# Kernel tuning notes

Measured on AMD Instinct MI355X. Metric: run time of the kernel, lower is better.

The kernel has to match this reference:

```python
import jax, jax.numpy as jnp
import numpy as np

CE_SLICES = [(1,10),(12,29),(30,33),(33,40),(40,64),(64,79),(79,84),(84,94),(94,96),(96,99),(99,105),(105,113),(116,122),(122,128),(128,151),(151,159),(160,165)]
MSE_COLS = [0,10,11,29,113,114,115,159,165,166,167]
BINS = 800
RATIO_JSD = 0.1  # stand-in for par.RATIO_JSD (not defined in source)
B = 262144


def setup_inputs() -> dict:
    key = jax.random.key(0)
    k1, k2, k3, k4 = jax.random.split(key, 4)
    data_encoded = jax.random.normal(k1, (B, 11), dtype=jnp.float32)
    data_decoded = jax.random.normal(k2, (B, 168), dtype=jnp.float32)
    data_true = jax.random.normal(k3, (B, 168), dtype=jnp.float32)
    # categorical blocks of data_true must be one-hot (nonzero-based decode)
    for j, (s, e) in enumerate(CE_SLICES):
        lab = jax.random.randint(jax.random.fold_in(k3, j), (B,), 0, e - s)
        data_true = data_true.at[:, s:e].set(jax.nn.one_hot(lab, e - s, dtype=jnp.float32))
    label_true = jax.random.randint(k4, (B, 1), 0, 2).astype(jnp.float32)
    return {"data_encoded": data_encoded, "data_decoded": data_decoded,
            "data_true": data_true, "label_true": label_true, "batch_size": B}


def _ce(logits, labels):
    # F.cross_entropy with mean reduction
    logp = jax.nn.log_softmax(logits, axis=-1)
    return -jnp.mean(jnp.take_along_axis(logp, labels[:, None], axis=1))


def _hist(x, mn, mx, mask):
    # torch.histc semantics: BINS equal bins on [mn, mx], top edge inclusive.
    t = (x - mn) / (mx - mn)
    idx = jnp.clip(jnp.floor(t * BINS).astype(jnp.int32), 0, BINS - 1)
    return jax.ops.segment_sum(mask, idx, num_segments=BINS)


def _kl(p, q, eps=1e-12):
    return jnp.sum(jnp.where(p > 0, p * jnp.log((p + eps) / (q + eps)), 0.0))


def reference(data_encoded, data_decoded, data_true, label_true, batch_size):
    # ---- MSE losses over 11 scalar columns (vectorized) ----
    cols = jnp.array(MSE_COLS)
    diff = data_decoded[:, cols] - data_true[:, cols]            # [B, 11]
    mse_loss = jnp.sum(jnp.mean(diff * diff, axis=0))

    # ---- 17 cross-entropy heads (labels decoded from one-hot blocks) ----
    ce_loss = jnp.float32(0.0)
    for s, e in CE_SLICES:
        labels = jnp.argmax(data_true[:, s:e], axis=1)           # == first nonzero for one-hot
        ce_loss = ce_loss + _ce(data_decoded[:, s:e], labels)

    # ---- JSD between male/female histograms of first 10 encoded dims ----
    combined = jnp.concatenate([data_encoded, label_true], axis=1)  # [B, 12]
    mn = jnp.min(combined, axis=0)
    mx = jnp.max(combined, axis=0)
    male = (combined[:, 11] == 0).astype(jnp.float32)
    female = (combined[:, 11] == 1).astype(jnp.float32)
    cols10 = combined[:, :10].T                                  # [10, B]
    hist = jax.vmap(_hist, in_axes=(0, 0, 0, None))              # [10, BINS]
    m_h = hist(cols10, mn[:10], mx[:10], male) / jnp.sum(male)
    f_h = hist(cols10, mn[:10], mx[:10], female) / jnp.sum(female)
    mid = 0.5 * (m_h + f_h)
    kld = 0.5 * (_kl(m_h, mid) + _kl(f_h, mid))                  # Jensen-Shannon divergence

    multi = (1.0 - RATIO_JSD) * (mse_loss + ce_loss) + RATIO_JSD * kld
    return jnp.stack([multi, mse_loss, ce_loss, RATIO_JSD * kld])
```

## Files before the change

### kernel.cpp

```cpp
#include <hip/hip_runtime.h>
#include <math.h>


#define BINS 800
#define NHCOLS 10
#define HBLK 256

#define MIN_OFF 0
#define MAX_OFF 16
#define CNT_OFF 32
#define MH_OFF  64
#define FH_OFF  8064
#define SUM2_OFF 16384
#define SUM2_CE  (SUM2_OFF + 2048)
#define WS_TOTAL_U32 20480

__device__ __forceinline__ unsigned f2ord(float f) {
  unsigned u = __float_as_uint(f);
  return (u & 0x80000000u) ? ~u : (u | 0x80000000u);
}
__device__ __forceinline__ float ord2f(unsigned e) {
  return __uint_as_float((e & 0x80000000u) ? (e & 0x7FFFFFFFu) : ~e);
}

__global__ void k_init(unsigned* __restrict__ ws) {
  int i = blockIdx.x * blockDim.x + threadIdx.x;
  if (i < WS_TOTAL_U32) ws[i] = (i < 11) ? 0xFFFFFFFFu : 0u;
}

__global__ __launch_bounds__(256) void k_minmax(const float* __restrict__ enc,
                                                const float* __restrict__ lab,
                                                unsigned* __restrict__ ws, int B) {
  const int tid    = blockIdx.x * blockDim.x + threadIdx.x;
  const int stride = gridDim.x * blockDim.x;
  const int c      = tid % 11;
  unsigned mn = 0xFFFFFFFFu, mx = 0u;
  const long long total = (long long)B * 11;
  for (long long i = tid; i < total; i += stride) {
    unsigned e = f2ord(enc[i]);
    mn = mn < e ? mn : e;
    mx = mx > e ? mx : e;
  }
  __shared__ unsigned smn[11], smx[11], scnt[2];
  if (threadIdx.x < 11) { smn[threadIdx.x] = 0xFFFFFFFFu; smx[threadIdx.x] = 0u; }
  if (threadIdx.x < 2)  scnt[threadIdx.x] = 0u;
  __syncthreads();
  atomicMin(&smn[c], mn);
  atomicMax(&smx[c], mx);
  unsigned m = 0, f = 0;
  for (int i = tid; i < B; i += stride) {
    float v = lab[i];
    m += (v == 0.0f);
    f += (v == 1.0f);
  }
  atomicAdd(&scnt[0], m);
  atomicAdd(&scnt[1], f);
  __syncthreads();
  if (threadIdx.x < 11) {
    atomicMin(&ws[MIN_OFF + threadIdx.x], smn[threadIdx.x]);
    atomicMax(&ws[MAX_OFF + threadIdx.x], smx[threadIdx.x]);
  }
  if (threadIdx.x == 11) atomicAdd(&ws[CNT_OFF + 0], scnt[0]);
  if (threadIdx.x == 12) atomicAdd(&ws[CNT_OFF + 1], scnt[1]);
}

__global__ __launch_bounds__(256) void k_hist(const float* __restrict__ enc,
                                              const float* __restrict__ lab,
                                              unsigned* __restrict__ ws, int B) {
  __shared__ unsigned h[2][NHCOLS * BINS];
  __shared__ float smn[NHCOLS], srng[NHCOLS];
  unsigned* hf = &h[0][0];
  for (int i = threadIdx.x; i < 2 * NHCOLS * BINS; i += blockDim.x) hf[i] = 0u;
  if (threadIdx.x < NHCOLS) {
    float lo = ord2f(ws[MIN_OFF + threadIdx.x]);
    float hi = ord2f(ws[MAX_OFF + threadIdx.x]);
    smn[threadIdx.x] = lo;
    srng[threadIdx.x] = hi - lo;
  }
  __syncthreads();
  const int sub    = (threadIdx.x >> 6) & 1;
  const int total  = B * 11;
  const int stride = HBLK * 256;
  const int qs     = stride / 11;
  const int rs     = stride % 11;
  int i = blockIdx.x * 256 + threadIdx.x;
  int r = i / 11;
  int c = i - r * 11;
  for (; i < total; i += stride) {
    if (c < NHCOLS) {
      float lv = lab[r];
      unsigned add = (lv == 0.0f) ? 1u : ((lv == 1.0f) ? 0x10000u : 0u);
      if (add) {
        float t = (enc[i] - smn[c]) / srng[c];
        int b = (int)floorf(t * 800.0f);
        b = b < 0 ? 0 : (b > BINS - 1 ? BINS - 1 : b);
        atomicAdd(&h[sub][c * BINS + b], add);
      }
    }
    r += qs; c += rs;
    if (c >= 11) { c -= 11; ++r; }
  }
  __syncthreads();
  for (int k = threadIdx.x; k < NHCOLS * BINS; k += blockDim.x) {
    unsigned v = h[0][k] + h[1][k];
    unsigned m = v & 0xFFFFu, f = v >> 16;
    if (m) atomicAdd(&ws[MH_OFF + k], m);
    if (f) atomicAdd(&ws[FH_OFF + k], f);
  }
}

__host__ __device__ constexpr int slice_of(int c) {
  return (c>=1&&c<10)?0:(c>=12&&c<29)?1:(c>=30&&c<33)?2:(c>=33&&c<40)?3:
         (c>=40&&c<64)?4:(c>=64&&c<79)?5:(c>=79&&c<84)?6:(c>=84&&c<94)?7:
         (c>=94&&c<96)?8:(c>=96&&c<99)?9:(c>=99&&c<105)?10:(c>=105&&c<113)?11:
         (c>=116&&c<122)?12:(c>=122&&c<128)?13:(c>=128&&c<151)?14:
         (c>=151&&c<159)?15:(c>=160&&c<165)?16:-1;
}
__host__ __device__ constexpr bool mse_of(int c) {
  return c==0||c==10||c==11||c==29||c==113||c==114||c==115||c==159||
         c==165||c==166||c==167;
}

template<int I, int K>
__device__ __forceinline__ void elem(const float (&d)[11][4], const float (&t)[11][4],
                                     float (&s)[17], float &dot, float &mse, int j) {
  constexpr int c0 = 16*I + K, c1 = c0+4, c2 = c0+8, c3 = c0+12;
  constexpr int cem = ((c0<168 && slice_of(c0)>=0)?1:0) |
                      ((c1<168 && slice_of(c1)>=0)?2:0) |
                      ((c2<168 && slice_of(c2)>=0)?4:0) |
                      ((c3<168 && slice_of(c3)>=0)?8:0);
  constexpr int msm = ((c0<168 && mse_of(c0))?1:0) | ((c1<168 && mse_of(c1))?2:0) |
                      ((c2<168 && mse_of(c2))?4:0) | ((c3<168 && mse_of(c3))?8:0);
  const float dv = d[I][K], tv = t[I][K];
  if constexpr (cem != 0) {
    float e = __expf(dv);
    if constexpr (cem & 1) s[slice_of(c0)] += (j == 0) ? e : 0.0f;
    if constexpr (cem & 2) s[slice_of(c1)] += (j == 1) ? e : 0.0f;
    if constexpr (cem & 4) s[slice_of(c2)] += (j == 2) ? e : 0.0f;
    if constexpr (cem & 8) s[slice_of(c3)] += (j == 3) ? e : 0.0f;
    dot += ((cem >> j) & 1) ? tv * dv : 0.0f;
  }
  if constexpr (msm != 0) {
    float df = dv - tv;
    mse += ((msm >> j) & 1) ? df * df : 0.0f;
  }
}

template<int I>
__device__ __forceinline__ void elem_row(const float (&d)[11][4], const float (&t)[11][4],
                                         float (&s)[17], float &dot, float &mse, int j) {
  elem<I,0>(d, t, s, dot, mse, j);
  elem<I,1>(d, t, s, dot, mse, j);
  elem<I,2>(d, t, s, dot, mse, j);
  elem<I,3>(d, t, s, dot, mse, j);
}

__global__ __launch_bounds__(256, 3) void k_main(const float* __restrict__ dec,
                                                 const float* __restrict__ tru,
                                                 float* __restrict__ wsf, int B) {
  const int lane = threadIdx.x & 63;
  const int wid  = threadIdx.x >> 6;
  const int j    = lane & 3;
  const int row  = blockIdx.x * 64 + (wid << 4) + (lane >> 2);
  const bool valid = row < B;
  const int rowc = valid ? row : (B - 1);

  float d[11][4], t[11][4];
  const float4* d4 = (const float4*)(dec + (size_t)rowc * 168);
  const float4* t4 = (const float4*)(tru + (size_t)rowc * 168);
#pragma unroll
  for (int i = 0; i < 11; ++i) {
    int w = 4 * i + j;
    w = w > 41 ? 41 : w;
    const float4 dv = d4[w];
    const float4 tv = t4[w];
    d[i][0] = dv.x; d[i][1] = dv.y; d[i][2] = dv.z; d[i][3] = dv.w;
    t[i][0] = tv.x; t[i][1] = tv.y; t[i][2] = tv.z; t[i][3] = tv.w;
  }
#pragma unroll
  for (int i = 0; i < 11; ++i) {
    asm volatile("" : "+v"(d[i][0]), "+v"(d[i][1]), "+v"(d[i][2]), "+v"(d[i][3]),
                      "+v"(t[i][0]), "+v"(t[i][1]), "+v"(t[i][2]), "+v"(t[i][3]));
  }

  float s[17];
#pragma unroll
  for (int k = 0; k < 17; ++k) s[k] = 0.0f;
  float dot = 0.0f, mse = 0.0f;

  elem_row<0>(d, t, s, dot, mse, j);
  elem_row<1>(d, t, s, dot, mse, j);
  elem_row<2>(d, t, s, dot, mse, j);
  elem_row<3>(d, t, s, dot, mse, j);
  elem_row<4>(d, t, s, dot, mse, j);
  elem_row<5>(d, t, s, dot, mse, j);
  elem_row<6>(d, t, s, dot, mse, j);
  elem_row<7>(d, t, s, dot, mse, j);
  elem_row<8>(d, t, s, dot, mse, j);
  elem_row<9>(d, t, s, dot, mse, j);
  elem_row<10>(d, t, s, dot, mse, j);

  dot += __shfl_xor(dot, 1, 64);
  dot += __shfl_xor(dot, 2, 64);
#pragma unroll
  for (int k = 0; k < 17; ++k) {
    s[k] += __shfl_xor(s[k], 1, 64);
    s[k] += __shfl_xor(s[k], 2, 64);
  }
  float ce = -dot;
#pragma unroll
  for (int k = 0; k < 17; ++k) ce += __logf(s[k]);

  ce  = (valid && j == 0) ? ce : 0.0f;
  mse = valid ? mse : 0.0f;

  __shared__ float sm[4], sc[4];
#pragma unroll
  for (int off = 32; off > 0; off >>= 1) {
    mse += __shfl_down(mse, off, 64);
    ce  += __shfl_down(ce, off, 64);
  }
  if (lane == 0) { sm[wid] = mse; sc[wid] = ce; }
  __syncthreads();
  if (threadIdx.x == 0) {
    const int slot = (blockIdx.x & 63) * 32;
    atomicAdd(&wsf[SUM2_OFF + slot], sm[0] + sm[1] + sm[2] + sm[3]);
    atomicAdd(&wsf[SUM2_CE  + slot], sc[0] + sc[1] + sc[2] + sc[3]);
  }
}

__global__ __launch_bounds__(256) void k_final(const unsigned* __restrict__ ws,
                                               float* __restrict__ out, int B) {
  const float* wsf = (const float*)ws;
  float male   = (float)ws[CNT_OFF + 0];
  float female = (float)ws[CNT_OFF + 1];
  float local = 0.0f;
  for (int i = threadIdx.x; i < NHCOLS * BINS; i += blockDim.x) {
    float mh  = (float)ws[MH_OFF + i] / male;
    float fh  = (float)ws[FH_OFF + i] / female;
    float mid = 0.5f * (mh + fh);
    if (mh > 0.0f) local += mh * logf((mh + 1e-12f) / (mid + 1e-12f));
    if (fh > 0.0f) local += fh * logf((fh + 1e-12f) / (mid + 1e-12f));
  }
  int lane = threadIdx.x & 63, wid = threadIdx.x >> 6;
  float msep = 0.0f, cep = 0.0f;
  if (threadIdx.x < 64) {
    msep = wsf[SUM2_OFF + threadIdx.x * 32];
    cep  = wsf[SUM2_CE  + threadIdx.x * 32];
  }
  __shared__ float s[4], sm2, sc2;
#pragma unroll
  for (int off = 32; off > 0; off >>= 1) {
    local += __shfl_down(local, off, 64);
    msep  += __shfl_down(msep, off, 64);
    cep   += __shfl_down(cep, off, 64);
  }
  if (lane == 0) s[wid] = local;
  if (threadIdx.x == 0) { sm2 = msep; sc2 = cep; }
  __syncthreads();
  if (threadIdx.x == 0) {
    float kld   = 0.5f * (s[0] + s[1] + s[2] + s[3]);
    float mse   = sm2 / (float)B;
    float ce    = sc2 / (float)B;
    float multi = 0.9f * (mse + ce) + 0.1f * kld;
    out[0] = multi;
    out[1] = mse;
    out[2] = ce;
    out[3] = 0.1f * kld;
  }
}

extern "C" void kernel_launch(void* const* d_in, const int* in_sizes, int n_in,
                              void* d_out, int out_size, void* d_ws, size_t ws_size,
                              hipStream_t stream) {
  (void)n_in; (void)out_size; (void)ws_size;
  const float* enc = (const float*)d_in[0];
  const float* dec = (const float*)d_in[1];
  const float* tru = (const float*)d_in[2];
  const float* lab = (const float*)d_in[3];
  const int B = in_sizes[3];
  unsigned* ws = (unsigned*)d_ws;
  float* out = (float*)d_out;

  hipLaunchKernelGGL(k_init, dim3((WS_TOTAL_U32 + 255) / 256), dim3(256), 0, stream, ws);
  hipLaunchKernelGGL(k_minmax, dim3(352), dim3(256), 0, stream, enc, lab, ws, B);
  hipLaunchKernelGGL(k_hist, dim3(HBLK), dim3(256), 0, stream, enc, lab, ws, B);
  hipLaunchKernelGGL(k_main, dim3((B + 63) / 64), dim3(256), 0, stream,
                     dec, tru, (float*)ws, B);
  hipLaunchKernelGGL(k_final, dim3(1), dim3(256), 0, stream, ws, out, B);
}
```

Before: 443.0 us.

## Remap main kernel to eight lanes per row and replace init kernel with memset

The main kernel now assigns eight lanes per row instead of four, so each thread holds 6 float4 vectors instead of 11. Column masks are rebuilt with constexpr helpers and the shuffle reductions gain one more stage. Launch bounds are raised to target four blocks per SIMD. The min-reduction is stored as a max over bitwise-inverted values, so an all-zero memset can replace the custom init kernel. The intent is lower register pressure, higher occupancy, more loads in flight, and one fewer kernel launch, at the cost of extra shuffles and more blocks.

After: 439.3 us. About the same (-0.8%).

```diff
diff --git a/kernel.cpp b/kernel.cpp
--- a/kernel.cpp
+++ b/kernel.cpp
@@ -15,17 +15,14 @@
 #define SUM2_CE  (SUM2_OFF + 2048)
 #define WS_TOTAL_U32 20480
 
+typedef float f4 __attribute__((ext_vector_type(4)));
+
 __device__ __forceinline__ unsigned f2ord(float f) {
   unsigned u = __float_as_uint(f);
   return (u & 0x80000000u) ? ~u : (u | 0x80000000u);
 }
 __device__ __forceinline__ float ord2f(unsigned e) {
   return __uint_as_float((e & 0x80000000u) ? (e & 0x7FFFFFFFu) : ~e);
-}
-
-__global__ void k_init(unsigned* __restrict__ ws) {
-  int i = blockIdx.x * blockDim.x + threadIdx.x;
-  if (i < WS_TOTAL_U32) ws[i] = (i < 11) ? 0xFFFFFFFFu : 0u;
 }
 
 __global__ __launch_bounds__(256) void k_minmax(const float* __restrict__ enc,
@@ -34,18 +31,19 @@
   const int tid    = blockIdx.x * blockDim.x + threadIdx.x;
   const int stride = gridDim.x * blockDim.x;
   const int c      = tid % 11;
-  unsigned mn = 0xFFFFFFFFu, mx = 0u;
+  unsigned mni = 0u, mx = 0u;
   const long long total = (long long)B * 11;
   for (long long i = tid; i < total; i += stride) {
     unsigned e = f2ord(enc[i]);
-    mn = mn < e ? mn : e;
-    mx = mx > e ? mx : e;
+    unsigned ei = ~e;
+    mni = mni > ei ? mni : ei;
+    mx  = mx  > e  ? mx  : e;
   }
   __shared__ unsigned smn[11], smx[11], scnt[2];
-  if (threadIdx.x < 11) { smn[threadIdx.x] = 0xFFFFFFFFu; smx[threadIdx.x] = 0u; }
+  if (threadIdx.x < 11) { smn[threadIdx.x] = 0u; smx[threadIdx.x] = 0u; }
   if (threadIdx.x < 2)  scnt[threadIdx.x] = 0u;
   __syncthreads();
-  atomicMin(&smn[c], mn);
+  atomicMax(&smn[c], mni);
   atomicMax(&smx[c], mx);
   unsigned m = 0, f = 0;
   for (int i = tid; i < B; i += stride) {
@@ -57,7 +55,7 @@
   atomicAdd(&scnt[1], f);
   __syncthreads();
   if (threadIdx.x < 11) {
-    atomicMin(&ws[MIN_OFF + threadIdx.x], smn[threadIdx.x]);
+    atomicMax(&ws[MIN_OFF + threadIdx.x], smn[threadIdx.x]);
     atomicMax(&ws[MAX_OFF + threadIdx.x], smx[threadIdx.x]);
   }
   if (threadIdx.x == 11) atomicAdd(&ws[CNT_OFF + 0], scnt[0]);
@@ -72,7 +70,7 @@
   unsigned* hf = &h[0][0];
   for (int i = threadIdx.x; i < 2 * NHCOLS * BINS; i += blockDim.x) hf[i] = 0u;
   if (threadIdx.x < NHCOLS) {
-    float lo = ord2f(ws[MIN_OFF + threadIdx.x]);
+    float lo = ord2f(~ws[MIN_OFF + threadIdx.x]);
     float hi = ord2f(ws[MAX_OFF + threadIdx.x]);
     smn[threadIdx.x] = lo;
     srng[threadIdx.x] = hi - lo;
@@ -120,34 +118,50 @@
   return c==0||c==10||c==11||c==29||c==113||c==114||c==115||c==159||
          c==165||c==166||c==167;
 }
+__host__ __device__ constexpr unsigned cem_of(int base) {
+  unsigned m = 0;
+  for (int jj = 0; jj < 8; ++jj) {
+    int c = base + 4 * jj;
+    if (c < 168 && slice_of(c) >= 0) m |= (1u << jj);
+  }
+  return m;
+}
+__host__ __device__ constexpr unsigned msm_of(int base) {
+  unsigned m = 0;
+  for (int jj = 0; jj < 8; ++jj) {
+    int c = base + 4 * jj;
+    if (c < 168 && mse_of(c)) m |= (1u << jj);
+  }
+  return m;
+}
 
 template<int I, int K>
-__device__ __forceinline__ void elem(const float (&d)[11][4], const float (&t)[11][4],
+__device__ __forceinline__ void elem(const f4 (&d)[6], const f4 (&t)[6],
                                      float (&s)[17], float &dot, float &mse, int j) {
-  constexpr int c0 = 16*I + K, c1 = c0+4, c2 = c0+8, c3 = c0+12;
-  constexpr int cem = ((c0<168 && slice_of(c0)>=0)?1:0) |
-                      ((c1<168 && slice_of(c1)>=0)?2:0) |
-                      ((c2<168 && slice_of(c2)>=0)?4:0) |
-                      ((c3<168 && slice_of(c3)>=0)?8:0);
-  constexpr int msm = ((c0<168 && mse_of(c0))?1:0) | ((c1<168 && mse_of(c1))?2:0) |
-                      ((c2<168 && mse_of(c2))?4:0) | ((c3<168 && mse_of(c3))?8:0);
+  constexpr int base = 32 * I + K;
+  constexpr unsigned cem = cem_of(base);
+  constexpr unsigned msm = msm_of(base);
   const float dv = d[I][K], tv = t[I][K];
   if constexpr (cem != 0) {
     float e = __expf(dv);
-    if constexpr (cem & 1) s[slice_of(c0)] += (j == 0) ? e : 0.0f;
-    if constexpr (cem & 2) s[slice_of(c1)] += (j == 1) ? e : 0.0f;
-    if constexpr (cem & 4) s[slice_of(c2)] += (j == 2) ? e : 0.0f;
-    if constexpr (cem & 8) s[slice_of(c3)] += (j == 3) ? e : 0.0f;
-    dot += ((cem >> j) & 1) ? tv * dv : 0.0f;
+    if constexpr (cem & 1u)   s[slice_of(base + 0)]  += (j == 0) ? e : 0.0f;
+    if constexpr (cem & 2u)   s[slice_of(base + 4)]  += (j == 1) ? e : 0.0f;
+    if constexpr (cem & 4u)   s[slice_of(base + 8)]  += (j == 2) ? e : 0.0f;
+    if constexpr (cem & 8u)   s[slice_of(base + 12)] += (j == 3) ? e : 0.0f;
+    if constexpr (cem & 16u)  s[slice_of(base + 16)] += (j == 4) ? e : 0.0f;
+    if constexpr (cem & 32u)  s[slice_of(base + 20)] += (j == 5) ? e : 0.0f;
+    if constexpr (cem & 64u)  s[slice_of(base + 24)] += (j == 6) ? e : 0.0f;
+    if constexpr (cem & 128u) s[slice_of(base + 28)] += (j == 7) ? e : 0.0f;
+    dot += ((cem >> j) & 1u) ? tv * dv : 0.0f;
   }
   if constexpr (msm != 0) {
     float df = dv - tv;
-    mse += ((msm >> j) & 1) ? df * df : 0.0f;
+    mse += ((msm >> j) & 1u) ? df * df : 0.0f;
   }
 }
 
 template<int I>
-__device__ __forceinline__ void elem_row(const float (&d)[11][4], const float (&t)[11][4],
+__device__ __forceinline__ void elem_row(const f4 (&d)[6], const f4 (&t)[6],
                                          float (&s)[17], float &dot, float &mse, int j) {
   elem<I,0>(d, t, s, dot, mse, j);
   elem<I,1>(d, t, s, dot, mse, j);
@@ -155,33 +169,28 @@
   elem<I,3>(d, t, s, dot, mse, j);
 }
 
-__global__ __launch_bounds__(256, 3) void k_main(const float* __restrict__ dec,
+__global__ __launch_bounds__(256, 4) void k_main(const float* __restrict__ dec,
                                                  const float* __restrict__ tru,
                                                  float* __restrict__ wsf, int B) {
   const int lane = threadIdx.x & 63;
   const int wid  = threadIdx.x >> 6;
-  const int j    = lane & 3;
-  const int row  = blockIdx.x * 64 + (wid << 4) + (lane >> 2);
+  const int j    = lane & 7;
+  const int row  = blockIdx.x * 32 + (wid << 3) + (lane >> 3);
   const bool valid = row < B;
   const int rowc = valid ? row : (B - 1);
 
-  float d[11][4], t[11][4];
-  const float4* d4 = (const float4*)(dec + (size_t)rowc * 168);
-  const float4* t4 = (const float4*)(tru + (size_t)rowc * 168);
-#pragma unroll
-  for (int i = 0; i < 11; ++i) {
-    int w = 4 * i + j;
-    w = w > 41 ? 41 : w;
-    const float4 dv = d4[w];
-    const float4 tv = t4[w];
-    d[i][0] = dv.x; d[i][1] = dv.y; d[i][2] = dv.z; d[i][3] = dv.w;
-    t[i][0] = tv.x; t[i][1] = tv.y; t[i][2] = tv.z; t[i][3] = tv.w;
-  }
-#pragma unroll
-  for (int i = 0; i < 11; ++i) {
-    asm volatile("" : "+v"(d[i][0]), "+v"(d[i][1]), "+v"(d[i][2]), "+v"(d[i][3]),
-                      "+v"(t[i][0]), "+v"(t[i][1]), "+v"(t[i][2]), "+v"(t[i][3]));
-  }
+  const f4* d4 = (const f4*)(dec + (size_t)rowc * 168);
+  const f4* t4 = (const f4*)(tru + (size_t)rowc * 168);
+  const int w5 = (40 + j) > 41 ? 41 : (40 + j);
+
+  f4 d[6], t[6];
+#pragma unroll
+  for (int i = 0; i < 5; ++i) {
+    d[i] = d4[8 * i + j];
+    t[i] = t4[8 * i + j];
+  }
+  d[5] = d4[w5];
+  t[5] = t4[w5];
 
   float s[17];
 #pragma unroll
@@ -194,18 +203,15 @@
   elem_row<3>(d, t, s, dot, mse, j);
   elem_row<4>(d, t, s, dot, mse, j);
   elem_row<5>(d, t, s, dot, mse, j);
-  elem_row<6>(d, t, s, dot, mse, j);
-  elem_row<7>(d, t, s, dot, mse, j);
-  elem_row<8>(d, t, s, dot, mse, j);
-  elem_row<9>(d, t, s, dot, mse, j);
-  elem_row<10>(d, t, s, dot, mse, j);
 
   dot += __shfl_xor(dot, 1, 64);
   dot += __shfl_xor(dot, 2, 64);
+  dot += __shfl_xor(dot, 4, 64);
 #pragma unroll
   for (int k = 0; k < 17; ++k) {
     s[k] += __shfl_xor(s[k], 1, 64);
     s[k] += __shfl_xor(s[k], 2, 64);
+    s[k] += __shfl_xor(s[k], 4, 64);
   }
   float ce = -dot;
 #pragma unroll
@@ -282,10 +288,10 @@
   unsigned* ws = (unsigned*)d_ws;
   float* out = (float*)d_out;
 
-  hipLaunchKernelGGL(k_init, dim3((WS_TOTAL_U32 + 255) / 256), dim3(256), 0, stream, ws);
+  hipMemsetAsync(ws, 0, WS_TOTAL_U32 * 4, stream);
   hipLaunchKernelGGL(k_minmax, dim3(352), dim3(256), 0, stream, enc, lab, ws, B);
   hipLaunchKernelGGL(k_hist, dim3(HBLK), dim3(256), 0, stream, enc, lab, ws, B);
-  hipLaunchKernelGGL(k_main, dim3((B + 63) / 64), dim3(256), 0, stream,
+  hipLaunchKernelGGL(k_main, dim3((B + 31) / 32), dim3(256), 0, stream,
                      dec, tru, (float*)ws, B);
   hipLaunchKernelGGL(k_final, dim3(1), dim3(256), 0, stream, ws, out, B);
 }
```
